# Optimization experiments

Hardware: AMD Instinct MI355X
Metric: run time of the kernel (lower is better)

The kernel has to match this reference:

```python
import jax, jax.numpy as jnp
import numpy as np


def setup_inputs() -> dict:
    key = jax.random.key(0)
    kq, kk, kv, kmask = jax.random.split(key, 4)
    B, H, L, D = 2, 16, 2048, 64
    q = jax.random.normal(kq, (B, H, L, D), dtype=jnp.float32)
    k = jax.random.normal(kk, (B, H, L, D), dtype=jnp.float32)
    v = jax.random.normal(kv, (B, H, L, D), dtype=jnp.float32)
    valid = jax.random.randint(kmask, (B, H, L, L), 0, 2, dtype=jnp.int32)
    scale = jnp.ones((), dtype=jnp.float32)  # typically 1/sqrt(D)
    return {"q": q, "k": k, "v": v, "valid": valid, "scale": scale}


def reference(q, k, v, valid, scale):
    # scores: [B, H, Lq, Lk]
    att_v = jnp.einsum('bhqd,bhkd->bhqk', q, k)
    att_v = att_v * scale
    att_v = att_v - jnp.max(att_v, axis=-1, keepdims=True)
    att_v = jnp.where(valid <= 0, -jnp.inf, att_v)
    att_w = jax.nn.softmax(att_v, axis=-1)
    # rows that are fully masked produce NaN -> zero them (matches torch masked_fill on isnan)
    att_w = jnp.where(jnp.isnan(att_w), jnp.zeros((), dtype=att_w.dtype), att_w)
    result = jnp.einsum('bhqk,bhkd->bhqd', att_w, v)
    return (result, att_w)
```

## Files before the change

kernel.cpp:

```cpp
#include <hip/hip_runtime.h>
#include <hip/hip_fp16.h>

#define L_    2048
#define D_    64
#define QT    64
#define NKT   32
#define PBP   72

typedef _Float16 half8  __attribute__((ext_vector_type(8)));
typedef _Float16 half4  __attribute__((ext_vector_type(4)));
typedef float    f32x4  __attribute__((ext_vector_type(4)));

__device__ __forceinline__ f32x4 mfma16f(half8 a, half8 b, f32x4 c) {
    return __builtin_amdgcn_mfma_f32_16x16x32_f16(a, b, c, 0, 0, 0);
}

__global__ __launch_bounds__(256)
void cvt_k(const float* __restrict__ Kg, _Float16* __restrict__ Kh)
{
    const int base = blockIdx.x * 1024 + threadIdx.x;
#pragma unroll
    for (int j = 0; j < 4; ++j) {
        const size_t c = (size_t)base + (size_t)j * 256;
        f32x4 x = ((const f32x4*)Kg)[c];
        half4 h;
#pragma unroll
        for (int e = 0; e < 4; ++e) h[e] = (_Float16)x[e];
        ((half4*)Kh)[c] = h;
    }
}

__global__ __launch_bounds__(256)
void tr_v(const float* __restrict__ Vg, _Float16* __restrict__ Vth)
{
    __shared__ float t[64][65];
    const int bh = blockIdx.x >> 5;
    const int kt = blockIdx.x & 31;
    const float* src = Vg + ((size_t)bh * L_ + (size_t)kt * 64) * D_;
    const int tid = threadIdx.x;
#pragma unroll
    for (int j = 0; j < 4; ++j) {
        const int k = j * 16 + (tid >> 4);
        const int d = (tid & 15) * 4;
        f32x4 x = *(const f32x4*)(src + k * 64 + d);
#pragma unroll
        for (int e = 0; e < 4; ++e) t[d + e][k] = x[e];
    }
    __syncthreads();
    _Float16* dst = Vth + (size_t)bh * 64 * L_ + (size_t)kt * 64;
#pragma unroll
    for (int j = 0; j < 4; ++j) {
        const int d = j * 16 + (tid >> 4);
        const int k = (tid & 15) * 4;
        half4 h;
#pragma unroll
        for (int e = 0; e < 4; ++e) h[e] = (_Float16)t[d][k + e];
        *(half4*)(dst + (size_t)d * L_ + k) = h;
    }
}

template<bool WS>
__global__ __launch_bounds__(256, 4)
void attn_fused(const float* __restrict__ Qg, const float* __restrict__ Kg,
                const float* __restrict__ Vg, const int* __restrict__ validg,
                const float* __restrict__ scaleg,
                const _Float16* __restrict__ Khg, const _Float16* __restrict__ Vthg,
                float* __restrict__ outR, float* __restrict__ outW)
{
    __shared__ __attribute__((aligned(16))) _Float16 Pbuf[64 * PBP];

    const int tid  = threadIdx.x;
    const int wv   = tid >> 6;
    const int lane = tid & 63;
    const int ln   = lane & 15;
    const int qd   = lane >> 4;

    const int bidx = blockIdx.x;
    const int bh   = (bidx & 7) * 4 + ((bidx >> 3) & 3);
    const int qt   = bidx >> 5;

    const float scale = scaleg[0];

    const float* Qb = Qg + ((size_t)bh * L_ + (size_t)qt * QT) * D_;
    const float* Kb = Kg + (size_t)bh * L_ * D_;
    const float* Vb = Vg + (size_t)bh * L_ * D_;
    const _Float16* Khb  = Khg  ? Khg  + (size_t)bh * L_ * D_ : nullptr;
    const _Float16* Vthb = Vthg ? Vthg + (size_t)bh * D_ * L_ : nullptr;
    const int*   Mb = validg + ((size_t)bh * L_ + (size_t)qt * QT) * (size_t)L_;
    float* Ob = outR + ((size_t)bh * L_ + (size_t)qt * QT) * D_;
    float* Wb = outW + ((size_t)bh * L_ + (size_t)qt * QT) * (size_t)L_;

    half8 aF[2];
    {
        const float* qrow = Qb + (size_t)(wv * 16 + ln) * D_;
#pragma unroll
        for (int f = 0; f < 2; ++f) {
            f32x4 x0 = *(const f32x4*)(qrow + f * 32 + qd * 8);
            f32x4 x1 = *(const f32x4*)(qrow + f * 32 + qd * 8 + 4);
            half8 h;
#pragma unroll
            for (int j = 0; j < 4; ++j) { h[j] = (_Float16)x0[j]; h[4 + j] = (_Float16)x1[j]; }
            aF[f] = h;
        }
    }

    auto kfrag = [&](int kt, int ct, half8& b0, half8& b1) {
        if constexpr (WS) {
            const _Float16* p = Khb + (size_t)(kt * 64 + ct * 16 + ln) * D_ + qd * 8;
            b0 = *(const half8*)p;
            b1 = *(const half8*)(p + 32);
        } else {
            const float* p = Kb + (size_t)(kt * 64 + ct * 16 + ln) * D_ + qd * 8;
            f32x4 x0 = *(const f32x4*)p;
            f32x4 x1 = *(const f32x4*)(p + 4);
            f32x4 y0 = *(const f32x4*)(p + 32);
            f32x4 y1 = *(const f32x4*)(p + 36);
#pragma unroll
            for (int j = 0; j < 4; ++j) {
                b0[j] = (_Float16)x0[j]; b0[4 + j] = (_Float16)x1[j];
                b1[j] = (_Float16)y0[j]; b1[4 + j] = (_Float16)y1[j];
            }
        }
    };

    auto vfrag = [&](int kt, int c2, half8& v0, half8& v1) {
        if constexpr (WS) {
            const _Float16* p = Vthb + (size_t)(c2 * 16 + ln) * L_ + kt * 64 + qd * 8;
            v0 = *(const half8*)p;
            v1 = *(const half8*)(p + 32);
        } else {
            const float* p = Vb + (size_t)(kt * 64 + qd * 8) * D_ + (c2 * 16 + ln);
#pragma unroll
            for (int j = 0; j < 8; ++j) v0[j] = (_Float16)p[j * 64];
            p += 32 * 64;
#pragma unroll
            for (int j = 0; j < 8; ++j) v1[j] = (_Float16)p[j * 64];
        }
    };

    int mv[16];
    const int* maskbase = Mb + (size_t)(wv * 16 + qd * 4) * L_ + ln;
    auto loadM = [&](int kt) {
#pragma unroll
        for (int ct = 0; ct < 4; ++ct)
#pragma unroll
            for (int r = 0; r < 4; ++r)
                mv[ct * 4 + r] = maskbase[(size_t)r * L_ + kt * 64 + ct * 16];
    };

    unsigned short* bitsSlab = (unsigned short*)Ob;

    float lsum[4] = {0.f, 0.f, 0.f, 0.f};
    loadM(0);
    for (int kt = 0; kt < NKT; ++kt) {
        half8 kb[4][2];
#pragma unroll
        for (int ct = 0; ct < 4; ++ct) kfrag(kt, ct, kb[ct][0], kb[ct][1]);
        unsigned bits = 0;
#pragma unroll
        for (int i = 0; i < 16; ++i) bits |= (mv[i] > 0 ? 1u : 0u) << i;
        if (kt + 1 < NKT) loadM(kt + 1);
        bitsSlab[kt * 256 + tid] = (unsigned short)bits;
#pragma unroll
        for (int ct = 0; ct < 4; ++ct) {
            f32x4 acc = {0.f, 0.f, 0.f, 0.f};
            acc = mfma16f(aF[0], kb[ct][0], acc);
            acc = mfma16f(aF[1], kb[ct][1], acc);
#pragma unroll
            for (int r = 0; r < 4; ++r) {
                float bit = (float)((bits >> (ct * 4 + r)) & 1u);
                lsum[r] += bit * __expf(acc[r] * scale);
            }
        }
    }

    float invl[4];
#pragma unroll
    for (int r = 0; r < 4; ++r) {
        float v = lsum[r];
        v += __shfl_xor(v, 1);
        v += __shfl_xor(v, 2);
        v += __shfl_xor(v, 4);
        v += __shfl_xor(v, 8);
        invl[r] = v > 0.f ? 1.f / v : 0.f;
    }

    asm volatile("s_waitcnt vmcnt(0)" ::: "memory");

    f32x4 accO[4];
#pragma unroll
    for (int i = 0; i < 4; ++i) accO[i] = (f32x4){0.f, 0.f, 0.f, 0.f};

    unsigned bcur = bitsSlab[tid];
    for (int kt = 0; kt < NKT; ++kt) {
        unsigned bnext = (kt + 1 < NKT) ? (unsigned)bitsSlab[(kt + 1) * 256 + tid] : 0u;
        const unsigned bits = bcur;
#pragma unroll
        for (int ct = 0; ct < 4; ++ct) {
            half8 b0, b1;
            kfrag(kt, ct, b0, b1);
            f32x4 acc = {0.f, 0.f, 0.f, 0.f};
            acc = mfma16f(aF[0], b0, acc);
            acc = mfma16f(aF[1], b1, acc);
#pragma unroll
            for (int r = 0; r < 4; ++r) {
                const int qrow = wv * 16 + qd * 4 + r;
                float bit = (float)((bits >> (ct * 4 + r)) & 1u);
                float p = bit * __expf(acc[r] * scale) * invl[r];
                Pbuf[qrow * PBP + ct * 16 + ln] = (_Float16)p;
            }
        }
        half8 p0 = *(const half8*)&Pbuf[(wv * 16 + ln) * PBP + qd * 8];
        half8 p1 = *(const half8*)&Pbuf[(wv * 16 + ln) * PBP + 32 + qd * 8];
        {
            float* wp = Wb + (size_t)(wv * 16 + ln) * L_ + kt * 64;
            f32x4 s0, s1, s2, s3;
#pragma unroll
            for (int j = 0; j < 4; ++j) {
                s0[j] = (float)p0[j];     s1[j] = (float)p0[4 + j];
                s2[j] = (float)p1[j];     s3[j] = (float)p1[4 + j];
            }
            *(f32x4*)(wp + qd * 8)          = s0;
            *(f32x4*)(wp + qd * 8 + 4)      = s1;
            *(f32x4*)(wp + 32 + qd * 8)     = s2;
            *(f32x4*)(wp + 32 + qd * 8 + 4) = s3;
        }
#pragma unroll
        for (int c2 = 0; c2 < 4; ++c2) {
            half8 v0, v1;
            vfrag(kt, c2, v0, v1);
            accO[c2] = mfma16f(p0, v0, accO[c2]);
            accO[c2] = mfma16f(p1, v1, accO[c2]);
        }
        bcur = bnext;
    }

    __syncthreads();

#pragma unroll
    for (int c2 = 0; c2 < 4; ++c2)
#pragma unroll
        for (int r = 0; r < 4; ++r)
            Ob[(size_t)(wv * 16 + qd * 4 + r) * D_ + (c2 * 16 + ln)] = accO[c2][r];
}

extern "C" void kernel_launch(void* const* d_in, const int* in_sizes, int n_in,
                              void* d_out, int out_size, void* d_ws, size_t ws_size,
                              hipStream_t stream) {
    const float* q     = (const float*)d_in[0];
    const float* k     = (const float*)d_in[1];
    const float* v     = (const float*)d_in[2];
    const int*   valid = (const int*)d_in[3];
    const float* scale = (const float*)d_in[4];

    float* out_res  = (float*)d_out;
    float* out_attw = out_res + (size_t)2 * 16 * L_ * D_;

    const size_t elems = (size_t)2 * 16 * L_ * D_;
    const size_t need  = 2 * elems * sizeof(_Float16);

    dim3 grid(2 * 16 * (L_ / QT));
    dim3 block(256);

    if (ws_size >= need && d_ws != nullptr) {
        _Float16* Kh  = (_Float16*)d_ws;
        _Float16* Vth = Kh + elems;
        cvt_k<<<dim3(1024), dim3(256), 0, stream>>>(k, Kh);
        tr_v <<<dim3(1024), dim3(256), 0, stream>>>(v, Vth);
        attn_fused<true><<<grid, block, 0, stream>>>(q, k, v, valid, scale, Kh, Vth,
                                                     out_res, out_attw);
    } else {
        attn_fused<false><<<grid, block, 0, stream>>>(q, k, v, valid, scale, nullptr, nullptr,
                                                      out_res, out_attw);
    }
}
```

Measured before the change: 1.238 ms.

## Split key range across wave pairs and halve query tile for more blocks

The query tile shrinks from 64 to 32 rows. The four waves in a block now form two row groups times two key halves, and each wave handles 16 of the 32 key tiles. Partial row sums are combined through shared memory before normalisation, and the partial PV accumulators are reduced through LDS before the final store. Launch bounds now ask for 8 blocks per CU to raise occupancy and double the grid size. The costs are extra syncs and LDS reduction, plus possible register pressure or spills under the tighter launch bound.

```diff
diff --git a/kernel.cpp b/kernel.cpp
--- a/kernel.cpp
+++ b/kernel.cpp
@@ -3,8 +3,8 @@
 
 #define L_    2048
 #define D_    64
-#define QT    64
-#define NKT   32
+#define QT    32
+#define NKTH  16
 #define PBP   72
 
 typedef _Float16 half8  __attribute__((ext_vector_type(8)));
@@ -60,7 +60,7 @@
 }
 
 template<bool WS>
-__global__ __launch_bounds__(256, 4)
+__global__ __launch_bounds__(256, 8)
 void attn_fused(const float* __restrict__ Qg, const float* __restrict__ Kg,
                 const float* __restrict__ Vg, const int* __restrict__ validg,
                 const float* __restrict__ scaleg,
@@ -68,9 +68,12 @@
                 float* __restrict__ outR, float* __restrict__ outW)
 {
     __shared__ __attribute__((aligned(16))) _Float16 Pbuf[64 * PBP];
+    __shared__ float psum[2][32];
 
     const int tid  = threadIdx.x;
     const int wv   = tid >> 6;
+    const int rg   = wv & 1;
+    const int kh   = wv >> 1;
     const int lane = tid & 63;
     const int ln   = lane & 15;
     const int qd   = lane >> 4;
@@ -92,7 +95,7 @@
 
     half8 aF[2];
     {
-        const float* qrow = Qb + (size_t)(wv * 16 + ln) * D_;
+        const float* qrow = Qb + (size_t)(rg * 16 + ln) * D_;
 #pragma unroll
         for (int f = 0; f < 2; ++f) {
             f32x4 x0 = *(const f32x4*)(qrow + f * 32 + qd * 8);
@@ -139,8 +142,9 @@
     };
 
     int mv[16];
-    const int* maskbase = Mb + (size_t)(wv * 16 + qd * 4) * L_ + ln;
-    auto loadM = [&](int kt) {
+    const int* maskbase = Mb + (size_t)(rg * 16 + qd * 4) * L_ + ln;
+    auto loadM = [&](int ktl) {
+        const int kt = kh * NKTH + ktl;
 #pragma unroll
         for (int ct = 0; ct < 4; ++ct)
 #pragma unroll
@@ -152,20 +156,20 @@
 
     float lsum[4] = {0.f, 0.f, 0.f, 0.f};
     loadM(0);
-    for (int kt = 0; kt < NKT; ++kt) {
-        half8 kb[4][2];
-#pragma unroll
-        for (int ct = 0; ct < 4; ++ct) kfrag(kt, ct, kb[ct][0], kb[ct][1]);
+    for (int ktl = 0; ktl < NKTH; ++ktl) {
+        const int kt = kh * NKTH + ktl;
         unsigned bits = 0;
 #pragma unroll
         for (int i = 0; i < 16; ++i) bits |= (mv[i] > 0 ? 1u : 0u) << i;
-        if (kt + 1 < NKT) loadM(kt + 1);
-        bitsSlab[kt * 256 + tid] = (unsigned short)bits;
+        if (ktl + 1 < NKTH) loadM(ktl + 1);
+        bitsSlab[ktl * 256 + tid] = (unsigned short)bits;
 #pragma unroll
         for (int ct = 0; ct < 4; ++ct) {
+            half8 b0, b1;
+            kfrag(kt, ct, b0, b1);
             f32x4 acc = {0.f, 0.f, 0.f, 0.f};
-            acc = mfma16f(aF[0], kb[ct][0], acc);
-            acc = mfma16f(aF[1], kb[ct][1], acc);
+            acc = mfma16f(aF[0], b0, acc);
+            acc = mfma16f(aF[1], b1, acc);
 #pragma unroll
             for (int r = 0; r < 4; ++r) {
                 float bit = (float)((bits >> (ct * 4 + r)) & 1u);
@@ -174,7 +178,7 @@
         }
     }
 
-    float invl[4];
+    float tot[4];
 #pragma unroll
     for (int r = 0; r < 4; ++r) {
         float v = lsum[r];
@@ -182,18 +186,28 @@
         v += __shfl_xor(v, 2);
         v += __shfl_xor(v, 4);
         v += __shfl_xor(v, 8);
-        invl[r] = v > 0.f ? 1.f / v : 0.f;
-    }
-
-    asm volatile("s_waitcnt vmcnt(0)" ::: "memory");
+        tot[r] = v;
+    }
+    if (ln == 0) {
+#pragma unroll
+        for (int r = 0; r < 4; ++r) psum[kh][rg * 16 + qd * 4 + r] = tot[r];
+    }
+    __syncthreads();
+    float invl[4];
+#pragma unroll
+    for (int r = 0; r < 4; ++r) {
+        float t = psum[0][rg * 16 + qd * 4 + r] + psum[1][rg * 16 + qd * 4 + r];
+        invl[r] = t > 0.f ? 1.f / t : 0.f;
+    }
 
     f32x4 accO[4];
 #pragma unroll
     for (int i = 0; i < 4; ++i) accO[i] = (f32x4){0.f, 0.f, 0.f, 0.f};
 
     unsigned bcur = bitsSlab[tid];
-    for (int kt = 0; kt < NKT; ++kt) {
-        unsigned bnext = (kt + 1 < NKT) ? (unsigned)bitsSlab[(kt + 1) * 256 + tid] : 0u;
+    for (int ktl = 0; ktl < NKTH; ++ktl) {
+        const int kt = kh * NKTH + ktl;
+        unsigned bnext = (ktl + 1 < NKTH) ? (unsigned)bitsSlab[(ktl + 1) * 256 + tid] : 0u;
         const unsigned bits = bcur;
 #pragma unroll
         for (int ct = 0; ct < 4; ++ct) {
@@ -204,16 +218,15 @@
             acc = mfma16f(aF[1], b1, acc);
 #pragma unroll
             for (int r = 0; r < 4; ++r) {
-                const int qrow = wv * 16 + qd * 4 + r;
                 float bit = (float)((bits >> (ct * 4 + r)) & 1u);
                 float p = bit * __expf(acc[r] * scale) * invl[r];
-                Pbuf[qrow * PBP + ct * 16 + ln] = (_Float16)p;
+                Pbuf[(wv * 16 + qd * 4 + r) * PBP + ct * 16 + ln] = (_Float16)p;
             }
         }
         half8 p0 = *(const half8*)&Pbuf[(wv * 16 + ln) * PBP + qd * 8];
         half8 p1 = *(const half8*)&Pbuf[(wv * 16 + ln) * PBP + 32 + qd * 8];
         {
-            float* wp = Wb + (size_t)(wv * 16 + ln) * L_ + kt * 64;
+            float* wp = Wb + (size_t)(rg * 16 + ln) * L_ + kt * 64;
             f32x4 s0, s1, s2, s3;
 #pragma unroll
             for (int j = 0; j < 4; ++j) {
@@ -235,13 +248,26 @@
         bcur = bnext;
     }
 
+    float* Obuf = (float*)&Pbuf[0];
     __syncthreads();
-
-#pragma unroll
-    for (int c2 = 0; c2 < 4; ++c2)
-#pragma unroll
-        for (int r = 0; r < 4; ++r)
-            Ob[(size_t)(wv * 16 + qd * 4 + r) * D_ + (c2 * 16 + ln)] = accO[c2][r];
+    if (kh == 1) {
+#pragma unroll
+        for (int c2 = 0; c2 < 4; ++c2)
+#pragma unroll
+            for (int r = 0; r < 4; ++r)
+                Obuf[(rg * 16 + qd * 4 + r) * 68 + c2 * 16 + ln] = accO[c2][r];
+    }
+    __syncthreads();
+    if (kh == 0) {
+#pragma unroll
+        for (int c2 = 0; c2 < 4; ++c2)
+#pragma unroll
+            for (int r = 0; r < 4; ++r) {
+                const int row = rg * 16 + qd * 4 + r;
+                float val = accO[c2][r] + Obuf[row * 68 + c2 * 16 + ln];
+                Ob[(size_t)row * D_ + (c2 * 16 + ln)] = val;
+            }
+    }
 }
 
 extern "C" void kernel_launch(void* const* d_in, const int* in_sizes, int n_in,
```

Result: slower. 1.300 ms (+5.1%).
